# Kernel optimization log

Hardware: AMD Instinct MI355X
Metric: run time of the kernel (lower is better)

The kernel has to match this reference:

```python
import jax, jax.numpy as jnp
import numpy as np

NEG_SLOPE = 0.2


def gat_conv(x, W, att_s, att_d, bias, src, dst, heads, out_c, concat):
    n = x.shape[0]
    h = (x @ W).reshape(n, heads, out_c)                      # [N,H,C]
    a_s = (h * att_s).sum(-1)                                 # [N,H]
    a_d = (h * att_d).sum(-1)                                 # [N,H]
    logits = jax.nn.leaky_relu(a_s[src] + a_d[dst], NEG_SLOPE)  # [E,H]
    # segment softmax over incoming edges of each dst node (per head)
    m = jax.ops.segment_max(logits, dst, num_segments=n)
    e = jnp.exp(logits - m[dst])
    denom = jax.ops.segment_sum(e, dst, num_segments=n)
    alpha = e / denom[dst]                                    # [E,H]
    msg = h[src] * alpha[:, :, None]                          # [E,H,C]
    out = jax.ops.segment_sum(msg, dst, num_segments=n)       # [N,H,C]
    out = out.reshape(n, heads * out_c) if concat else out.mean(axis=1)
    return out + bias


def setup_inputs() -> dict:
    key = jax.random.key(0)
    ks = jax.random.split(key, 9)
    N, IN, OUT, E = 100000, 256, 40, 1600000
    return {
        "x": jax.random.normal(ks[0], (N, IN), jnp.float32),
        "edge_index": jax.random.randint(ks[1], (2, E), 0, N, jnp.int32),
        "W1": jax.random.normal(ks[2], (IN, 64), jnp.float32) * (1.0 / np.sqrt(IN)),
        "att_src1": jax.random.normal(ks[3], (8, 8), jnp.float32) * 0.1,
        "att_dst1": jax.random.normal(ks[4], (8, 8), jnp.float32) * 0.1,
        "b1": jnp.zeros((64,), jnp.float32),
        "W2": jax.random.normal(ks[5], (64, OUT), jnp.float32) * (1.0 / 8.0),
        "att_src2": jax.random.normal(ks[6], (1, OUT), jnp.float32) * 0.1,
        "att_dst2": jax.random.normal(ks[7], (1, OUT), jnp.float32) * 0.1,
        "b2": jnp.zeros((OUT,), jnp.float32),
    }


def reference(x, edge_index, W1, att_src1, att_dst1, b1, W2, att_src2, att_dst2, b2):
    n = x.shape[0]
    loop = jnp.arange(n, dtype=edge_index.dtype)
    src = jnp.concatenate([edge_index[0], loop])  # self-loops (PyG default)
    dst = jnp.concatenate([edge_index[1], loop])
    h = gat_conv(x, W1, att_src1, att_dst1, b1, src, dst, heads=8, out_c=8, concat=True)
    h = jax.nn.relu(h)
    out = gat_conv(h, W2, att_src2, att_dst2, b2, src, dst, heads=1, out_c=W2.shape[1], concat=True)
    return jax.nn.log_softmax(out, axis=1)
```

## Files before the change

### kernel.cpp

```cpp
#include <hip/hip_runtime.h>


#define L_IN   256
#define L_C1   64
#define L_H1   8
#define L_OUT  40
#define BCAP   5120

typedef __attribute__((ext_vector_type(8))) short short8;
typedef __attribute__((ext_vector_type(4))) float f32x4;

__device__ __forceinline__ float leaky(float x){ return fmaxf(x, 0.2f*x); }
__device__ __forceinline__ unsigned f2bf(float f){
  unsigned u = __float_as_uint(f);
  return (u + 0x7fffu + ((u >> 16) & 1u)) >> 16;
}
__device__ __forceinline__ float bflo(unsigned u){ return __uint_as_float(u << 16); }
__device__ __forceinline__ float bfhi(unsigned u){ return __uint_as_float(u & 0xffff0000u); }

__global__ __launch_bounds__(256) void prep_w1(const float* __restrict__ W1,
                                               ushort* __restrict__ wt,
                                               int* __restrict__ gcur, int NB){
  const int t = threadIdx.x;
  if (blockIdx.x == 4){
    for (int i = t; i < NB; i += 256) gcur[i] = 0;
    return;
  }
  __shared__ float ws[64][65];
  const int kb = blockIdx.x;
  #pragma unroll
  for (int i = 0; i < 16; ++i){
    int idx = t + i*256;
    ws[idx >> 6][idx & 63] = W1[(size_t)(kb*64 + (idx >> 6))*64 + (idx & 63)];
  }
  __syncthreads();
  int c  = t >> 2;
  int j0 = (t & 3) * 16;
  ushort tmp[16];
  #pragma unroll
  for (int j = 0; j < 16; ++j) tmp[j] = (ushort)f2bf(ws[j0 + j][c]);
  uint4* dst = (uint4*)(wt + (size_t)c*256 + kb*64 + j0);
  dst[0] = *(uint4*)&tmp[0];
  dst[1] = *(uint4*)&tmp[8];
}

__global__ __launch_bounds__(256) void bin_scatter(const int* __restrict__ esrc,
    const int* __restrict__ edst, int* __restrict__ gcur,
    unsigned* __restrict__ binned, int E, int NB){
  __shared__ int hist[512], rbase[512], cur[512];
  const int t  = threadIdx.x;
  const int e0 = blockIdx.x * 4096;
  hist[t] = 0; hist[t+256] = 0; cur[t] = 0; cur[t+256] = 0;
  __syncthreads();
  int sv[16], dv[16];
  const bool full = (e0 + 4096 <= E);
  if (full){
    #pragma unroll
    for (int j = 0; j < 4; ++j){
      int p4 = (e0 >> 2) + j*256 + t;
      int4 s4 = ((const int4*)esrc)[p4];
      int4 d4 = ((const int4*)edst)[p4];
      sv[4*j+0]=s4.x; sv[4*j+1]=s4.y; sv[4*j+2]=s4.z; sv[4*j+3]=s4.w;
      dv[4*j+0]=d4.x; dv[4*j+1]=d4.y; dv[4*j+2]=d4.z; dv[4*j+3]=d4.w;
      atomicAdd(&hist[d4.x >> 8], 1); atomicAdd(&hist[d4.y >> 8], 1);
      atomicAdd(&hist[d4.z >> 8], 1); atomicAdd(&hist[d4.w >> 8], 1);
    }
  } else {
    #pragma unroll
    for (int j = 0; j < 16; ++j){
      int idx = e0 + j*256 + t;
      if (idx < E){
        sv[j] = esrc[idx]; dv[j] = edst[idx];
        atomicAdd(&hist[dv[j] >> 8], 1);
      } else dv[j] = -1;
    }
  }
  __syncthreads();
  if (hist[t])                   rbase[t]     = atomicAdd(&gcur[t],     hist[t]);
  if (t+256 < NB && hist[t+256]) rbase[t+256] = atomicAdd(&gcur[t+256], hist[t+256]);
  __syncthreads();
  #pragma unroll
  for (int j = 0; j < 16; ++j){
    if (dv[j] >= 0){
      int b = dv[j] >> 8;
      int off = rbase[b] + atomicAdd(&cur[b], 1);
      if (off < BCAP)
        binned[(size_t)b*BCAP + off] =
          (unsigned)sv[j] | ((unsigned)(dv[j] & 255) << 17);
    }
  }
}

__global__ __launch_bounds__(256) void csr_gemm1(
    const unsigned* __restrict__ binned, const int* __restrict__ gcur,
    int2* __restrict__ nodeptr, int* __restrict__ csr, int NBK,
    const float* __restrict__ x, const ushort* __restrict__ wt,
    const float* __restrict__ atts, const float* __restrict__ attd,
    unsigned char* __restrict__ h1f, float* __restrict__ as1, float* __restrict__ ad1,
    int n, int ntiles, int npb)
{
  __shared__ __align__(16) char smem[43008];
  const int t   = threadIdx.x;
  const int bid = blockIdx.x;

  if (bid < NBK){
    unsigned* ebuf = (unsigned*)smem;
    int* cnt  = (int*)(smem + BCAP*4);
    int* pref = cnt + 256;
    int* cur  = pref + 256;
    const int b = bid;
    int ne = gcur[b]; if (ne > BCAP) ne = BCAP;
    const int base = b * BCAP;
    cnt[t] = 0; cur[t] = 0;
    __syncthreads();
    for (int i = t; i < ne; i += 256){
      unsigned e = binned[base + i];
      ebuf[i] = e;
      atomicAdd(&cnt[(e >> 17) & 255u], 1);
    }
    __syncthreads();
    pref[t] = cnt[t];
    __syncthreads();
    for (int off = 1; off < 256; off <<= 1){
      int a = (t >= off) ? pref[t-off] : 0;
      __syncthreads();
      pref[t] += a;
      __syncthreads();
    }
    int excl = pref[t] - cnt[t];
    __syncthreads();
    pref[t] = excl;
    int d = (b << 8) + t;
    if (d < n) nodeptr[d] = make_int2(base + excl, cnt[t]);
    __syncthreads();
    for (int i = t; i < ne; i += 256){
      unsigned e = ebuf[i];
      int ln = (int)((e >> 17) & 255u);
      int pos = base + pref[ln] + atomicAdd(&cur[ln], 1);
      csr[pos] = (int)(e & 0x1FFFFu);
    }
    return;
  }

  ushort (*ws)[264] = (ushort(*)[264])(smem);
  ushort (*hs)[72]  = (ushort(*)[72]) (smem + 33792);
  const int wv = t >> 6;
  const int ln = t & 63;
  const int fr = ln & 15;
  const int fq = ln >> 4;

  #pragma unroll
  for (int i = 0; i < 8; ++i){
    int idx = t + i*256;
    int row = idx >> 5, c8 = idx & 31;
    *(uint4*)&ws[row][c8*8] = *(const uint4*)(wt + (size_t)row*256 + c8*8);
  }
  __syncthreads();

  for (int tile = bid - NBK; tile < ntiles; tile += npb){
    const int rb = tile * 64;
    const int ar = rb + wv*16 + fr;
    const bool rv = ar < n;
    const float* xr = x + (size_t)(rv ? ar : 0) * L_IN;

    f32x4 acc[4];
    #pragma unroll
    for (int cb = 0; cb < 4; ++cb) acc[cb] = (f32x4){0.f,0.f,0.f,0.f};

    #pragma unroll
    for (int kk = 0; kk < 8; ++kk){
      const int k0 = kk*32 + fq*8;
      float4 a0 = make_float4(0.f,0.f,0.f,0.f), a1 = a0;
      if (rv){
        a0 = *(const float4*)(xr + k0);
        a1 = *(const float4*)(xr + k0 + 4);
      }
      uint4 au;
      au.x = f2bf(a0.x) | (f2bf(a0.y) << 16);
      au.y = f2bf(a0.z) | (f2bf(a0.w) << 16);
      au.z = f2bf(a1.x) | (f2bf(a1.y) << 16);
      au.w = f2bf(a1.z) | (f2bf(a1.w) << 16);
      short8 a = *(short8*)&au;
      #pragma unroll
      for (int cb = 0; cb < 4; ++cb){
        short8 b = *(const short8*)&ws[cb*16 + fr][k0];
        acc[cb] = __builtin_amdgcn_mfma_f32_16x16x32_bf16(a, b, acc[cb], 0, 0, 0);
      }
    }

    #pragma unroll
    for (int cb = 0; cb < 4; ++cb)
      #pragma unroll
      for (int r = 0; r < 4; ++r)
        hs[wv*16 + fq*4 + r][cb*16 + fr] = (ushort)f2bf(acc[cb][r]);

    #pragma unroll
    for (int i = 0; i < 2; ++i){
      int task = ln + i*64;
      int lrow = task >> 3;
      int sub  = task & 7;
      int row  = rb + wv*16 + lrow;
      if (row < n){
        uint4 u = *(const uint4*)&hs[wv*16 + lrow][sub*8];
        float v0=bflo(u.x), v1=bfhi(u.x), v2=bflo(u.y), v3=bfhi(u.y);
        float v4=bflo(u.z), v5=bfhi(u.z), v6=bflo(u.w), v7=bfhi(u.w);
        int d0 = __builtin_amdgcn_cvt_pk_fp8_f32(v0, v1, 0, false);
        d0 = __builtin_amdgcn_cvt_pk_fp8_f32(v2, v3, d0, true);
        int d1 = __builtin_amdgcn_cvt_pk_fp8_f32(v4, v5, 0, false);
        d1 = __builtin_amdgcn_cvt_pk_fp8_f32(v6, v7, d1, true);
        *(uint2*)(h1f + (size_t)row*L_C1 + sub*8) = make_uint2((unsigned)d0, (unsigned)d1);
        const float* sa = atts + sub*8;
        const float* da = attd + sub*8;
        float ds = v0*sa[0]+v1*sa[1]+v2*sa[2]+v3*sa[3]+v4*sa[4]+v5*sa[5]+v6*sa[6]+v7*sa[7];
        float dd = v0*da[0]+v1*da[1]+v2*da[2]+v3*da[3]+v4*da[4]+v5*da[5]+v6*da[6]+v7*da[7];
        as1[(size_t)row*L_H1 + sub] = ds;
        ad1[(size_t)row*L_H1 + sub] = dd;
      }
    }
  }
}

__global__ __launch_bounds__(256) void agg1_kernel(
    const int2* __restrict__ nodeptr, const int* __restrict__ csr,
    const unsigned char* __restrict__ h1f, const float* __restrict__ as1,
    const float* __restrict__ ad1, const float* __restrict__ b1,
    ushort* __restrict__ hrb, int n)
{
  int wid  = (blockIdx.x*blockDim.x + threadIdx.x) >> 6;
  int lane = threadIdx.x & 63;
  if (wid >= n) return;
  int2 np  = nodeptr[wid];
  int beg  = np.x;
  int degt = np.y + 1;

  const int h  = lane & 7;
  const int eg = lane >> 3;
  const int cq = lane & 15;
  const int eq = lane >> 4;
  const int hw = cq >> 1;

  float adn = ad1[(size_t)wid*L_H1 + h];
  float a0 = 0.f, a1 = 0.f, a2 = 0.f, a3 = 0.f, sp = 0.f;

  #define A1_ACC(U, WE)                                                    \
    { auto lo_ = __builtin_amdgcn_cvt_pk_f32_fp8((U), false);              \
      auto hi_ = __builtin_amdgcn_cvt_pk_f32_fp8((U), true);               \
      a0 += (WE)*lo_[0]; a1 += (WE)*lo_[1];                                \
      a2 += (WE)*hi_[0]; a3 += (WE)*hi_[1]; }

  if (degt <= 16){
    int i0 = eg, i1 = 8 + eg;
    int s0 = (i0 < degt-1) ? csr[beg + i0] : wid;
    int s1 = (i1 < degt-1) ? csr[beg + i1] : wid;
    float r0 = as1[(size_t)s0*L_H1 + h];
    float r1 = as1[(size_t)s1*L_H1 + h];
    int se00 = __shfl(s0, eq*8),     se01 = __shfl(s0, (4+eq)*8);
    int se10 = __shfl(s1, eq*8),     se11 = __shfl(s1, (4+eq)*8);
    unsigned u00 = *(const unsigned*)(h1f + (size_t)se00*L_C1 + cq*4);
    unsigned u01 = *(const unsigned*)(h1f + (size_t)se01*L_C1 + cq*4);
    unsigned u10 = *(const unsigned*)(h1f + (size_t)se10*L_C1 + cq*4);
    unsigned u11 = *(const unsigned*)(h1f + (size_t)se11*L_C1 + cq*4);
    float w0 = (i0 < degt) ? __expf(leaky(r0 + adn)) : 0.f;
    float w1 = (i1 < degt) ? __expf(leaky(r1 + adn)) : 0.f;
    sp = w0 + w1;
    float we00 = __shfl(w0, eq*8 + hw), we01 = __shfl(w0, (4+eq)*8 + hw);
    float we10 = __shfl(w1, eq*8 + hw), we11 = __shfl(w1, (4+eq)*8 + hw);
    A1_ACC(u00, we00) A1_ACC(u01, we01) A1_ACC(u10, we10) A1_ACC(u11, we11)
  } else if (degt <= 24){
    int i0 = eg, i1 = 8 + eg, i2 = 16 + eg;
    int s0 = (i0 < degt-1) ? csr[beg + i0] : wid;
    int s1 = (i1 < degt-1) ? csr[beg + i1] : wid;
    int s2 = (i2 < degt-1) ? csr[beg + i2] : wid;
    float r0 = as1[(size_t)s0*L_H1 + h];
    float r1 = as1[(size_t)s1*L_H1 + h];
    float r2 = as1[(size_t)s2*L_H1 + h];
    int se00 = __shfl(s0, eq*8), se01 = __shfl(s0, (4+eq)*8);
    int se10 = __shfl(s1, eq*8), se11 = __shfl(s1, (4+eq)*8);
    int se20 = __shfl(s2, eq*8), se21 = __shfl(s2, (4+eq)*8);
    unsigned u00 = *(const unsigned*)(h1f + (size_t)se00*L_C1 + cq*4);
    unsigned u01 = *(const unsigned*)(h1f + (size_t)se01*L_C1 + cq*4);
    unsigned u10 = *(const unsigned*)(h1f + (size_t)se10*L_C1 + cq*4);
    unsigned u11 = *(const unsigned*)(h1f + (size_t)se11*L_C1 + cq*4);
    unsigned u20 = *(const unsigned*)(h1f + (size_t)se20*L_C1 + cq*4);
    unsigned u21 = *(const unsigned*)(h1f + (size_t)se21*L_C1 + cq*4);
    float w0 = (i0 < degt) ? __expf(leaky(r0 + adn)) : 0.f;
    float w1 = (i1 < degt) ? __expf(leaky(r1 + adn)) : 0.f;
    float w2 = (i2 < degt) ? __expf(leaky(r2 + adn)) : 0.f;
    sp = w0 + w1 + w2;
    float we00 = __shfl(w0, eq*8 + hw), we01 = __shfl(w0, (4+eq)*8 + hw);
    float we10 = __shfl(w1, eq*8 + hw), we11 = __shfl(w1, (4+eq)*8 + hw);
    float we20 = __shfl(w2, eq*8 + hw), we21 = __shfl(w2, (4+eq)*8 + hw);
    A1_ACC(u00, we00) A1_ACC(u01, we01)
    A1_ACC(u10, we10) A1_ACC(u11, we11)
    A1_ACC(u20, we20) A1_ACC(u21, we21)
  } else {
    const int ngrp = (degt + 7) >> 3;
    for (int g = 0; g < ngrp; ++g){
      int i_ = g*8 + eg;
      int sg = (i_ < degt-1) ? csr[beg + i_] : wid;
      float rr = as1[(size_t)sg*L_H1 + h];
      int sea = __shfl(sg, eq*8), seb = __shfl(sg, (4+eq)*8);
      unsigned ua = *(const unsigned*)(h1f + (size_t)sea*L_C1 + cq*4);
      unsigned ub = *(const unsigned*)(h1f + (size_t)seb*L_C1 + cq*4);
      float wg = (i_ < degt) ? __expf(leaky(rr + adn)) : 0.f;
      sp += wg;
      float wea = __shfl(wg, eq*8 + hw), web = __shfl(wg, (4+eq)*8 + hw);
      A1_ACC(ua, wea) A1_ACC(ub, web)
    }
  }
  #undef A1_ACC

  #pragma unroll
  for (int off = 8; off < 64; off <<= 1) sp += __shfl_xor(sp, off);
  float rinv = 1.0f / __shfl(sp, hw);
  a0 += __shfl_xor(a0, 16); a0 += __shfl_xor(a0, 32);
  a1 += __shfl_xor(a1, 16); a1 += __shfl_xor(a1, 32);
  a2 += __shfl_xor(a2, 16); a2 += __shfl_xor(a2, 32);
  a3 += __shfl_xor(a3, 16); a3 += __shfl_xor(a3, 32);
  if (lane < 16){
    float4 bv = *(const float4*)&b1[cq*4];
    float r0 = fmaxf(a0*rinv + bv.x, 0.f);
    float r1 = fmaxf(a1*rinv + bv.y, 0.f);
    float r2 = fmaxf(a2*rinv + bv.z, 0.f);
    float r3 = fmaxf(a3*rinv + bv.w, 0.f);
    uint2 o;
    o.x = f2bf(r0) | (f2bf(r1) << 16);
    o.y = f2bf(r2) | (f2bf(r3) << 16);
    *(uint2*)(hrb + (size_t)wid*L_C1 + cq*4) = o;
  }
}

__global__ __launch_bounds__(256) void gemm2_kernel(
    const ushort* __restrict__ hrb, const float* __restrict__ W2,
    const float* __restrict__ atts2, const float* __restrict__ attd2,
    ushort* __restrict__ h2b, float* __restrict__ as2, float* __restrict__ ad2, int n)
{
  __shared__ float w2s[64*40];
  const int t = threadIdx.x;
  for (int i = t; i < 64*40; i += 256) w2s[i] = W2[i];
  __syncthreads();
  int row = blockIdx.x*256 + t;
  if (row >= n) return;

  uint4 rv[8];
  #pragma unroll
  for (int q = 0; q < 8; ++q)
    rv[q] = *(const uint4*)(hrb + (size_t)row*L_C1 + q*8);

  f32x4 acc4[10];
  #pragma unroll
  for (int j = 0; j < 10; ++j) acc4[j] = (f32x4){0.f,0.f,0.f,0.f};

  #pragma unroll
  for (int q = 0; q < 8; ++q){
    unsigned uu[4] = {rv[q].x, rv[q].y, rv[q].z, rv[q].w};
    #pragma unroll
    for (int d = 0; d < 4; ++d){
      int k = q*8 + d*2;
      float v0 = bflo(uu[d]), v1 = bfhi(uu[d]);
      const f32x4* w0 = (const f32x4*)&w2s[k*40];
      const f32x4* w1 = (const f32x4*)&w2s[(k+1)*40];
      #pragma unroll
      for (int j = 0; j < 10; ++j) acc4[j] += v0*w0[j] + v1*w1[j];
    }
  }

  float acc[40];
  #pragma unroll
  for (int j = 0; j < 10; ++j){
    acc[4*j+0]=acc4[j][0]; acc[4*j+1]=acc4[j][1];
    acc[4*j+2]=acc4[j][2]; acc[4*j+3]=acc4[j][3];
  }
  float ps = 0.f, pd = 0.f;
  #pragma unroll
  for (int j = 0; j < 40; ++j){ ps += acc[j]*atts2[j]; pd += acc[j]*attd2[j]; }
  unsigned pk[20];
  #pragma unroll
  for (int q = 0; q < 20; ++q) pk[q] = f2bf(acc[2*q]) | (f2bf(acc[2*q+1]) << 16);
  uint4* dst = (uint4*)(h2b + (size_t)row*L_OUT);
  #pragma unroll
  for (int q = 0; q < 5; ++q) dst[q] = make_uint4(pk[4*q],pk[4*q+1],pk[4*q+2],pk[4*q+3]);
  as2[row] = ps;
  ad2[row] = pd;
}

__global__ __launch_bounds__(256) void agg2_kernel(
    const int2* __restrict__ nodeptr, const int* __restrict__ csr,
    const ushort* __restrict__ h2b, const float* __restrict__ as2,
    const float* __restrict__ ad2, const float* __restrict__ b2,
    float* __restrict__ out, int n)
{
  int wid  = (blockIdx.x*blockDim.x + threadIdx.x) >> 6;
  int lane = threadIdx.x & 63;
  if (wid >= n) return;
  int2 np  = nodeptr[wid];
  int beg  = np.x;
  int degt = np.y + 1;

  const int eidx = (lane < 60) ? (lane / 20) : 0;
  const int cq   = (lane < 60) ? (lane % 20) : 0;

  float adn = ad2[wid];
  float ax = 0.f, ay = 0.f, sp = 0.f;

  if (degt <= 64){
    int i = lane;
    int src = (i < degt-1) ? csr[beg + i] : wid;
    float raw = as2[src];
    #define A2_LD(K, SE, U)                                                \
      { int e_ = 3*(K) + eidx;                                             \
        int es_ = (e_ < 64) ? e_ : 63;                                     \
        SE = es_;                                                          \
        int s_ = __shfl(src, es_);                                         \
        U = *(const unsigned*)(h2b + (size_t)s_*L_OUT + cq*2); }
    #define A2_FM(K, SE, U, W)                                             \
      { int e_ = 3*(K) + eidx;                                             \
        float we_ = __shfl((W), SE);                                       \
        we_ = (e_ < degt) ? we_ : 0.f;                                     \
        ax += we_ * bflo(U);                                               \
        ay += we_ * bfhi(U); }
    if (degt <= 18){
      int e0,e1,e2,e3,e4,e5; unsigned u0,u1,u2,u3,u4,u5;
      A2_LD(0,e0,u0) A2_LD(1,e1,u1) A2_LD(2,e2,u2)
      A2_LD(3,e3,u3) A2_LD(4,e4,u4) A2_LD(5,e5,u5)
      float l = (i < degt) ? leaky(raw + adn) : -1e30f;
      float w = __expf(l); sp = w;
      A2_FM(0,e0,u0,w) A2_FM(1,e1,u1,w) A2_FM(2,e2,u2,w)
      A2_FM(3,e3,u3,w) A2_FM(4,e4,u4,w) A2_FM(5,e5,u5,w)
    } else if (degt <= 27){
      int e0,e1,e2,e3,e4,e5,e6,e7,e8;
      unsigned u0,u1,u2,u3,u4,u5,u6,u7,u8;
      A2_LD(0,e0,u0) A2_LD(1,e1,u1) A2_LD(2,e2,u2)
      A2_LD(3,e3,u3) A2_LD(4,e4,u4) A2_LD(5,e5,u5)
      A2_LD(6,e6,u6) A2_LD(7,e7,u7) A2_LD(8,e8,u8)
      float l = (i < degt) ? leaky(raw + adn) : -1e30f;
      float w = __expf(l); sp = w;
      A2_FM(0,e0,u0,w) A2_FM(1,e1,u1,w) A2_FM(2,e2,u2,w)
      A2_FM(3,e3,u3,w) A2_FM(4,e4,u4,w) A2_FM(5,e5,u5,w)
      A2_FM(6,e6,u6,w) A2_FM(7,e7,u7,w) A2_FM(8,e8,u8,w)
    } else if (degt <= 36){
      int e0,e1,e2,e3,e4,e5,e6,e7,e8,e9,e10,e11;
      unsigned u0,u1,u2,u3,u4,u5,u6,u7,u8,u9,u10,u11;
      A2_LD(0,e0,u0) A2_LD(1,e1,u1) A2_LD(2,e2,u2)
      A2_LD(3,e3,u3) A2_LD(4,e4,u4) A2_LD(5,e5,u5)
      A2_LD(6,e6,u6) A2_LD(7,e7,u7) A2_LD(8,e8,u8)
      A2_LD(9,e9,u9) A2_LD(10,e10,u10) A2_LD(11,e11,u11)
      float l = (i < degt) ? leaky(raw + adn) : -1e30f;
      float w = __expf(l); sp = w;
      A2_FM(0,e0,u0,w) A2_FM(1,e1,u1,w) A2_FM(2,e2,u2,w)
      A2_FM(3,e3,u3,w) A2_FM(4,e4,u4,w) A2_FM(5,e5,u5,w)
      A2_FM(6,e6,u6,w) A2_FM(7,e7,u7,w) A2_FM(8,e8,u8,w)
      A2_FM(9,e9,u9,w) A2_FM(10,e10,u10,w) A2_FM(11,e11,u11,w)
    } else {
      float l = (i < degt) ? leaky(raw + adn) : -1e30f;
      float w = __expf(l); sp = w;
      for (int e0 = 0; e0 < degt; e0 += 9){
        #pragma unroll
        for (int st = 0; st < 3; ++st){
          int e  = e0 + st*3 + eidx;
          int es = (e < 64) ? e : 63;
          float we = __shfl(w,   es);
          int   se = __shfl(src, es);
          we = (e < degt) ? we : 0.f;
          unsigned u = *(const unsigned*)(h2b + (size_t)se*L_OUT + cq*2);
          ax += we * bflo(u);
          ay += we * bfhi(u);
        }
      }
    }
    #undef A2_LD
    #undef A2_FM
  } else {
    const int ngrp = (degt + 63) >> 6;
    for (int g = 0; g < ngrp; ++g){
      int i = g*64 + lane;
      int src = (i < degt-1) ? csr[beg + i] : wid;
      float l = (i < degt) ? leaky(as2[src] + adn) : -1e30f;
      float w = __expf(l);
      sp += w;
      int cnt = degt - g*64; if (cnt > 64) cnt = 64;
      for (int e0 = 0; e0 < cnt; e0 += 9){
        #pragma unroll
        for (int st = 0; st < 3; ++st){
          int e  = e0 + st*3 + eidx;
          int es = (e < 64) ? e : 63;
          float we = __shfl(w,   es);
          int   se = __shfl(src, es);
          we = (e < cnt) ? we : 0.f;
          unsigned u = *(const unsigned*)(h2b + (size_t)se*L_OUT + cq*2);
          ax += we * bflo(u);
          ay += we * bfhi(u);
        }
      }
    }
  }

  #pragma unroll
  for (int off = 1; off < 64; off <<= 1) sp += __shfl_xor(sp, off);
  float rinv = 1.0f / sp;

  float ax0 = __shfl(ax, cq), ax1 = __shfl(ax, cq+20), ax2 = __shfl(ax, cq+40);
  float ay0 = __shfl(ay, cq), ay1 = __shfl(ay, cq+20), ay2 = __shfl(ay, cq+40);
  float axs = (ax0 + ax1) + ax2;
  float ays = (ay0 + ay1) + ay2;

  bool act = (lane < 20);
  float o0 = axs*rinv + b2[cq*2];
  float o1 = ays*rinv + b2[cq*2+1];
  float mx = act ? fmaxf(o0, o1) : -1e30f;
  #pragma unroll
  for (int off = 1; off < 32; off <<= 1) mx = fmaxf(mx, __shfl_xor(mx, off));
  float ex = act ? (__expf(o0 - mx) + __expf(o1 - mx)) : 0.f;
  #pragma unroll
  for (int off = 1; off < 32; off <<= 1) ex += __shfl_xor(ex, off);
  float lse = mx + __logf(ex);
  if (act){
    float2 r = make_float2(o0 - lse, o1 - lse);
    *(float2*)(out + (size_t)wid*L_OUT + cq*2) = r;
  }
}

extern "C" void kernel_launch(void* const* d_in, const int* in_sizes, int n_in,
                              void* d_out, int out_size, void* d_ws, size_t ws_size,
                              hipStream_t stream)
{
  const float* x    = (const float*)d_in[0];
  const int*   ei   = (const int*)  d_in[1];
  const float* W1   = (const float*)d_in[2];
  const float* as1w = (const float*)d_in[3];
  const float* ad1w = (const float*)d_in[4];
  const float* b1   = (const float*)d_in[5];
  const float* W2   = (const float*)d_in[6];
  const float* as2w = (const float*)d_in[7];
  const float* ad2w = (const float*)d_in[8];
  const float* b2   = (const float*)d_in[9];

  const int N = in_sizes[0] / L_IN;
  const int E = in_sizes[1] / 2;
  const int NB = (N + 255) >> 8;
  const int NSC = (E + 4095) / 4096;
  const int NT1 = (N + 63) / 64;
  const int NPB = (NT1 < 768) ? NT1 : 768;
  const int* esrc = ei;
  const int* edst = ei + E;
  float* out = (float*)d_out;

  char* w = (char*)d_ws;
  auto alloc = [&](size_t bytes)->char*{
    char* p = w; w += (bytes + 255) & ~size_t(255); return p;
  };
  unsigned char* h1f = (unsigned char*)alloc((size_t)N*L_C1);
  float*  as1  = (float*) alloc((size_t)N*L_H1*4);
  float*  ad1  = (float*) alloc((size_t)N*L_H1*4);
  size_t union_sz = (size_t)N*L_C1*2 + (size_t)N*L_OUT*2;
  if (union_sz < (size_t)NB*BCAP*4) union_sz = (size_t)NB*BCAP*4;
  char*  ub    = alloc(union_sz);
  ushort* hrb  = (ushort*)ub;
  ushort* h2b  = (ushort*)(ub + (size_t)N*L_C1*2);
  unsigned* binned = (unsigned*)ub;
  float*  as2  = (float*) alloc((size_t)N*4);
  float*  ad2  = (float*) alloc((size_t)N*4);
  ushort* wt   = (ushort*)alloc((size_t)64*256*2);
  int2*  nodeptr=(int2*)  alloc((size_t)N*8);
  int*   csr   = (int*)   alloc((size_t)NB*BCAP*4);
  int*   gcur  = (int*)   alloc((size_t)NB*4);

  prep_w1     <<<5,          256, 0, stream>>>(W1, wt, gcur, NB);
  bin_scatter <<<NSC,        256, 0, stream>>>(esrc, edst, gcur, binned, E, NB);
  csr_gemm1   <<<NB + NPB,   256, 0, stream>>>(binned, gcur, nodeptr, csr, NB,
                                               x, wt, as1w, ad1w, h1f, as1, ad1,
                                               N, NT1, NPB);
  agg1_kernel <<<(N+3)/4,    256, 0, stream>>>(nodeptr, csr, h1f, as1, ad1, b1, hrb, N);
  gemm2_kernel<<<(N+255)/256,256, 0, stream>>>(hrb, W2, as2w, ad2w, h2b, as2, ad2, N);
  agg2_kernel <<<(N+3)/4,    256, 0, stream>>>(nodeptr, csr, h2b, as2, ad2, b2, out, N);
}
```

Before: 161.6 us.

## Split GEMM1 across both graph-build phases so it overlaps binning and CSR

Merges the edge binning kernel into the GEMM1 kernel and splits the GEMM1 row tiles into two halves. The first launch runs binning blocks alongside the first half of the GEMM tiles, and the second launch runs CSR build blocks alongside the second half. The goal is to hide the latency-bound, atomic-heavy graph construction behind the compute-bound GEMM inside the same launches. The cost is one more launch and a fixed 768-block GEMM grid per phase, which may leave tiles unevenly spread across blocks.

```diff
diff --git a/kernel.cpp b/kernel.cpp
--- a/kernel.cpp
+++ b/kernel.cpp
@@ -44,100 +44,101 @@
   dst[1] = *(uint4*)&tmp[8];
 }
 
-__global__ __launch_bounds__(256) void bin_scatter(const int* __restrict__ esrc,
-    const int* __restrict__ edst, int* __restrict__ gcur,
-    unsigned* __restrict__ binned, int E, int NB){
-  __shared__ int hist[512], rbase[512], cur[512];
-  const int t  = threadIdx.x;
-  const int e0 = blockIdx.x * 4096;
-  hist[t] = 0; hist[t+256] = 0; cur[t] = 0; cur[t+256] = 0;
-  __syncthreads();
-  int sv[16], dv[16];
-  const bool full = (e0 + 4096 <= E);
-  if (full){
-    #pragma unroll
-    for (int j = 0; j < 4; ++j){
-      int p4 = (e0 >> 2) + j*256 + t;
-      int4 s4 = ((const int4*)esrc)[p4];
-      int4 d4 = ((const int4*)edst)[p4];
-      sv[4*j+0]=s4.x; sv[4*j+1]=s4.y; sv[4*j+2]=s4.z; sv[4*j+3]=s4.w;
-      dv[4*j+0]=d4.x; dv[4*j+1]=d4.y; dv[4*j+2]=d4.z; dv[4*j+3]=d4.w;
-      atomicAdd(&hist[d4.x >> 8], 1); atomicAdd(&hist[d4.y >> 8], 1);
-      atomicAdd(&hist[d4.z >> 8], 1); atomicAdd(&hist[d4.w >> 8], 1);
-    }
-  } else {
-    #pragma unroll
-    for (int j = 0; j < 16; ++j){
-      int idx = e0 + j*256 + t;
-      if (idx < E){
-        sv[j] = esrc[idx]; dv[j] = edst[idx];
-        atomicAdd(&hist[dv[j] >> 8], 1);
-      } else dv[j] = -1;
-    }
-  }
-  __syncthreads();
-  if (hist[t])                   rbase[t]     = atomicAdd(&gcur[t],     hist[t]);
-  if (t+256 < NB && hist[t+256]) rbase[t+256] = atomicAdd(&gcur[t+256], hist[t+256]);
-  __syncthreads();
-  #pragma unroll
-  for (int j = 0; j < 16; ++j){
-    if (dv[j] >= 0){
-      int b = dv[j] >> 8;
-      int off = rbase[b] + atomicAdd(&cur[b], 1);
-      if (off < BCAP)
-        binned[(size_t)b*BCAP + off] =
-          (unsigned)sv[j] | ((unsigned)(dv[j] & 255) << 17);
-    }
-  }
-}
-
-__global__ __launch_bounds__(256) void csr_gemm1(
-    const unsigned* __restrict__ binned, const int* __restrict__ gcur,
-    int2* __restrict__ nodeptr, int* __restrict__ csr, int NBK,
+__global__ __launch_bounds__(256) void build_gemm1(
+    int PHASE, int NROLE,
+    const int* __restrict__ esrc, const int* __restrict__ edst,
+    int* __restrict__ gcur, unsigned* __restrict__ binned, int E, int NB,
+    int2* __restrict__ nodeptr, int* __restrict__ csr,
     const float* __restrict__ x, const ushort* __restrict__ wt,
     const float* __restrict__ atts, const float* __restrict__ attd,
     unsigned char* __restrict__ h1f, float* __restrict__ as1, float* __restrict__ ad1,
-    int n, int ntiles, int npb)
+    int n, int tile0, int tile1, int npb)
 {
   __shared__ __align__(16) char smem[43008];
   const int t   = threadIdx.x;
   const int bid = blockIdx.x;
 
-  if (bid < NBK){
-    unsigned* ebuf = (unsigned*)smem;
-    int* cnt  = (int*)(smem + BCAP*4);
-    int* pref = cnt + 256;
-    int* cur  = pref + 256;
-    const int b = bid;
-    int ne = gcur[b]; if (ne > BCAP) ne = BCAP;
-    const int base = b * BCAP;
-    cnt[t] = 0; cur[t] = 0;
-    __syncthreads();
-    for (int i = t; i < ne; i += 256){
-      unsigned e = binned[base + i];
-      ebuf[i] = e;
-      atomicAdd(&cnt[(e >> 17) & 255u], 1);
-    }
-    __syncthreads();
-    pref[t] = cnt[t];
-    __syncthreads();
-    for (int off = 1; off < 256; off <<= 1){
-      int a = (t >= off) ? pref[t-off] : 0;
-      __syncthreads();
-      pref[t] += a;
-      __syncthreads();
-    }
-    int excl = pref[t] - cnt[t];
-    __syncthreads();
-    pref[t] = excl;
-    int d = (b << 8) + t;
-    if (d < n) nodeptr[d] = make_int2(base + excl, cnt[t]);
-    __syncthreads();
-    for (int i = t; i < ne; i += 256){
-      unsigned e = ebuf[i];
-      int ln = (int)((e >> 17) & 255u);
-      int pos = base + pref[ln] + atomicAdd(&cur[ln], 1);
-      csr[pos] = (int)(e & 0x1FFFFu);
+  if (bid < NROLE){
+    if (PHASE == 1){
+      int* hist  = (int*)smem;
+      int* rbase = hist + 512;
+      int* cur   = rbase + 512;
+      const int e0 = bid * 4096;
+      hist[t] = 0; hist[t+256] = 0; cur[t] = 0; cur[t+256] = 0;
+      __syncthreads();
+      int sv[16], dv[16];
+      const bool full = (e0 + 4096 <= E);
+      if (full){
+        #pragma unroll
+        for (int j = 0; j < 4; ++j){
+          int p4 = (e0 >> 2) + j*256 + t;
+          int4 s4 = ((const int4*)esrc)[p4];
+          int4 d4 = ((const int4*)edst)[p4];
+          sv[4*j+0]=s4.x; sv[4*j+1]=s4.y; sv[4*j+2]=s4.z; sv[4*j+3]=s4.w;
+          dv[4*j+0]=d4.x; dv[4*j+1]=d4.y; dv[4*j+2]=d4.z; dv[4*j+3]=d4.w;
+          atomicAdd(&hist[d4.x >> 8], 1); atomicAdd(&hist[d4.y >> 8], 1);
+          atomicAdd(&hist[d4.z >> 8], 1); atomicAdd(&hist[d4.w >> 8], 1);
+        }
+      } else {
+        #pragma unroll
+        for (int j = 0; j < 16; ++j){
+          int idx = e0 + j*256 + t;
+          if (idx < E){
+            sv[j] = esrc[idx]; dv[j] = edst[idx];
+            atomicAdd(&hist[dv[j] >> 8], 1);
+          } else dv[j] = -1;
+        }
+      }
+      __syncthreads();
+      if (hist[t])                   rbase[t]     = atomicAdd(&gcur[t],     hist[t]);
+      if (t+256 < NB && hist[t+256]) rbase[t+256] = atomicAdd(&gcur[t+256], hist[t+256]);
+      __syncthreads();
+      #pragma unroll
+      for (int j = 0; j < 16; ++j){
+        if (dv[j] >= 0){
+          int b = dv[j] >> 8;
+          int off = rbase[b] + atomicAdd(&cur[b], 1);
+          if (off < BCAP)
+            binned[(size_t)b*BCAP + off] =
+              (unsigned)sv[j] | ((unsigned)(dv[j] & 255) << 17);
+        }
+      }
+    } else {
+      unsigned* ebuf = (unsigned*)smem;
+      int* cnt  = (int*)(smem + BCAP*4);
+      int* pref = cnt + 256;
+      int* cur  = pref + 256;
+      const int b = bid;
+      int ne = gcur[b]; if (ne > BCAP) ne = BCAP;
+      const int base = b * BCAP;
+      cnt[t] = 0; cur[t] = 0;
+      __syncthreads();
+      for (int i = t; i < ne; i += 256){
+        unsigned e = binned[base + i];
+        ebuf[i] = e;
+        atomicAdd(&cnt[(e >> 17) & 255u], 1);
+      }
+      __syncthreads();
+      pref[t] = cnt[t];
+      __syncthreads();
+      for (int off = 1; off < 256; off <<= 1){
+        int a = (t >= off) ? pref[t-off] : 0;
+        __syncthreads();
+        pref[t] += a;
+        __syncthreads();
+      }
+      int excl = pref[t] - cnt[t];
+      __syncthreads();
+      pref[t] = excl;
+      int d = (b << 8) + t;
+      if (d < n) nodeptr[d] = make_int2(base + excl, cnt[t]);
+      __syncthreads();
+      for (int i = t; i < ne; i += 256){
+        unsigned e = ebuf[i];
+        int ln = (int)((e >> 17) & 255u);
+        int pos = base + pref[ln] + atomicAdd(&cur[ln], 1);
+        csr[pos] = (int)(e & 0x1FFFFu);
+      }
     }
     return;
   }
@@ -157,7 +158,7 @@
   }
   __syncthreads();
 
-  for (int tile = bid - NBK; tile < ntiles; tile += npb){
+  for (int tile = tile0 + (bid - NROLE); tile < tile1; tile += npb){
     const int rb = tile * 64;
     const int ar = rb + wv*16 + fr;
     const bool rv = ar < n;
@@ -540,7 +541,8 @@
   const int NB = (N + 255) >> 8;
   const int NSC = (E + 4095) / 4096;
   const int NT1 = (N + 63) / 64;
-  const int NPB = (NT1 < 768) ? NT1 : 768;
+  const int HALF = (NT1 + 1) / 2;
+  const int G1 = 768;
   const int* esrc = ei;
   const int* edst = ei + E;
   float* out = (float*)d_out;
@@ -565,11 +567,15 @@
   int*   csr   = (int*)   alloc((size_t)NB*BCAP*4);
   int*   gcur  = (int*)   alloc((size_t)NB*4);
 
-  prep_w1     <<<5,          256, 0, stream>>>(W1, wt, gcur, NB);
-  bin_scatter <<<NSC,        256, 0, stream>>>(esrc, edst, gcur, binned, E, NB);
-  csr_gemm1   <<<NB + NPB,   256, 0, stream>>>(binned, gcur, nodeptr, csr, NB,
+  prep_w1    <<<5,           256, 0, stream>>>(W1, wt, gcur, NB);
+  build_gemm1<<<NSC + G1,    256, 0, stream>>>(1, NSC, esrc, edst, gcur, binned,
+                                               E, NB, nodeptr, csr,
                                                x, wt, as1w, ad1w, h1f, as1, ad1,
-                                               N, NT1, NPB);
+                                               N, 0, HALF, G1);
+  build_gemm1<<<NB + G1,     256, 0, stream>>>(2, NB, esrc, edst, gcur, binned,
+                                               E, NB, nodeptr, csr,
+                                               x, wt, as1w, ad1w, h1f, as1, ad1,
+                                               N, HALF, NT1, G1);
   agg1_kernel <<<(N+3)/4,    256, 0, stream>>>(nodeptr, csr, h1f, as1, ad1, b1, hrb, N);
   gemm2_kernel<<<(N+255)/256,256, 0, stream>>>(hrb, W2, as2w, ad2w, h2b, as2, ad2, N);
   agg2_kernel <<<(N+3)/4,    256, 0, stream>>>(nodeptr, csr, h2b, as2, ad2, b2, out, N);
```

Result: no change. 164.4 us (+1.7%).
